# Kernel tuning notes

Hardware: AMD Instinct MI355X
Metric: run time of the kernel (lower is better)

The kernel has to match this reference:

```python
import jax, jax.numpy as jnp
import numpy as np

B = 1024
P = 9            # patch_length
D = 2700         # d_model = input_dims = 30*30*3, num_heads=1 so d_k = D
DFF = 512
EPS = 1e-5


def setup_inputs() -> dict:
    key = jax.random.key(0)
    ks = jax.random.split(key, 32)
    s = 0.02
    inp = {
        "state": jax.random.normal(ks[0], (B, P * D), jnp.float32),
        "H1": jax.random.normal(ks[1], (B, P, DFF), jnp.float32),
        "H2": jax.random.normal(ks[2], (B, P, DFF), jnp.float32),
        # main projections: (in, out) layout for x @ W
        "Wq": jax.random.normal(ks[3], (D, D), jnp.float32) * s,
        "bq": jnp.zeros((D,), jnp.float32),
        "Wk": jax.random.normal(ks[4], (D, D), jnp.float32) * s,
        "bk": jnp.zeros((D,), jnp.float32),
        "Wv": jax.random.normal(ks[5], (D, D), jnp.float32) * s,
        "bv": jnp.zeros((D,), jnp.float32),
        # aux modulation projections from dff -> d_model
        "WC1q": jax.random.normal(ks[6], (DFF, D), jnp.float32) * s,
        "bC1q": jnp.zeros((D,), jnp.float32),
        "WC1k": jax.random.normal(ks[7], (DFF, D), jnp.float32) * s,
        "bC1k": jnp.zeros((D,), jnp.float32),
        "WC1v": jax.random.normal(ks[8], (DFF, D), jnp.float32) * s,
        "bC1v": jnp.zeros((D,), jnp.float32),
        "WC2q": jax.random.normal(ks[9], (DFF, D), jnp.float32) * s,
        "bC2q": jnp.zeros((D,), jnp.float32),
        "WC2k": jax.random.normal(ks[10], (DFF, D), jnp.float32) * s,
        "bC2k": jnp.zeros((D,), jnp.float32),
        "WC2v": jax.random.normal(ks[11], (DFF, D), jnp.float32) * s,
        "bC2v": jnp.zeros((D,), jnp.float32),
        # LayerNorm (norm1) affine params
        "gamma": jnp.ones((D,), jnp.float32),
        "beta": jnp.zeros((D,), jnp.float32),
    }
    return inp


def _layernorm(x, gamma, beta):
    mu = jnp.mean(x, axis=-1, keepdims=True)
    var = jnp.mean(jnp.square(x - mu), axis=-1, keepdims=True)
    return (x - mu) * jax.lax.rsqrt(var + EPS) * gamma + beta


def reference(state, H1, H2, Wq, bq, Wk, bk, Wv, bv,
              WC1q, bC1q, WC1k, bC1k, WC1v, bC1v,
              WC2q, bC2q, WC2k, bC2k, WC2v, bC2v,
              gamma, beta):
    x = state.reshape(-1, P, D)  # (B, 9, 2700)
    # elementwise-modulated Q/K/V (num_heads == 1)
    q = (x @ Wq + bq) * ((H1 @ WC1q + bC1q) + (H2 @ WC2q + bC2q))
    k = (x @ Wk + bk) * ((H1 @ WC1k + bC1k) + (H2 @ WC2k + bC2k))
    v = (x @ Wv + bv) * ((H1 @ WC1v + bC1v) + (H2 @ WC2v + bC2v))
    scale = 1.0 / jnp.sqrt(jnp.asarray(D, jnp.float32))
    scores = jnp.einsum("bqd,bkd->bqk", q, k) * scale  # (B, 9, 9)
    A = jax.nn.softmax(scores, axis=-1)
    attn = jnp.einsum("bqk,bkd->bqd", A, v)
    Z1 = x + attn  # dropout is identity in eval
    return _layernorm(Z1, gamma, beta)
```

## Files before the change

### kernel.cpp

```cpp
#include <hip/hip_runtime.h>
#include <stdint.h>


#define MROWS  9216
#define NCOLS  8192
#define KP1    2752
#define KP2    1024
#define DMODEL 2700

typedef __bf16 bf16x8 __attribute__((ext_vector_type(8)));
typedef float  f32x4  __attribute__((ext_vector_type(4)));

__device__ __forceinline__ float b2f(unsigned short u) {
  union { unsigned int u; float f; } v; v.u = ((unsigned int)u) << 16; return v.f;
}
__device__ __forceinline__ unsigned short f2b(float f) {
  union { float f; unsigned int u; } v; v.f = f;
  unsigned int r = v.u + 0x7FFFu + ((v.u >> 16) & 1u);
  return (unsigned short)(r >> 16);
}

__device__ __forceinline__ void gl2lds16(const void* g, void* l) {
  __builtin_amdgcn_global_load_lds(
      (const __attribute__((address_space(1))) void*)g,
      (__attribute__((address_space(3))) void*)l, 16, 0, 0);
}


__global__ void cvt_x(const float* __restrict__ src, unsigned short* __restrict__ dst) {
  int t = blockIdx.x * 256 + threadIdx.x;
  int r = t / 344;
  int c8 = (t - r * 344) * 8;
  const float* row = src + (size_t)r * DMODEL;
  unsigned int w[4];
  if (c8 + 8 <= DMODEL) {
    float4 a = *(const float4*)(row + c8);
    float4 b = *(const float4*)(row + c8 + 4);
    w[0] = (unsigned int)f2b(a.x) | ((unsigned int)f2b(a.y) << 16);
    w[1] = (unsigned int)f2b(a.z) | ((unsigned int)f2b(a.w) << 16);
    w[2] = (unsigned int)f2b(b.x) | ((unsigned int)f2b(b.y) << 16);
    w[3] = (unsigned int)f2b(b.z) | ((unsigned int)f2b(b.w) << 16);
  } else {
#pragma unroll
    for (int h = 0; h < 4; h++) {
      int c0 = c8 + 2 * h, c1 = c8 + 2 * h + 1;
      unsigned int lo = (c0 < DMODEL) ? f2b(row[c0]) : 0u;
      unsigned int hi = (c1 < DMODEL) ? f2b(row[c1]) : 0u;
      w[h] = lo | (hi << 16);
    }
  }
  *(uint4*)(dst + (size_t)t * 8) = make_uint4(w[0], w[1], w[2], w[3]);
}

__global__ void cvt_h(const float* __restrict__ H1, const float* __restrict__ H2,
                      unsigned short* __restrict__ dst) {
  int t = blockIdx.x * 256 + threadIdx.x;
  int r = t >> 7, c8 = (t & 127) * 8;
  const float* row = (c8 < 512) ? (H1 + (size_t)r * 512 + c8)
                                : (H2 + (size_t)r * 512 + (c8 - 512));
  float4 a = *(const float4*)(row);
  float4 b = *(const float4*)(row + 4);
  unsigned int w0 = (unsigned int)f2b(a.x) | ((unsigned int)f2b(a.y) << 16);
  unsigned int w1 = (unsigned int)f2b(a.z) | ((unsigned int)f2b(a.w) << 16);
  unsigned int w2 = (unsigned int)f2b(b.x) | ((unsigned int)f2b(b.y) << 16);
  unsigned int w3 = (unsigned int)f2b(b.z) | ((unsigned int)f2b(b.w) << 16);
  *(uint4*)(dst + (size_t)t * 8) = make_uint4(w0, w1, w2, w3);
}

__global__ void cvt_wqkv(const float* __restrict__ Wq, const float* __restrict__ Wk,
                         const float* __restrict__ Wv, unsigned short* __restrict__ Wt) {
  __shared__ float tile[64][65];
  const int k0 = blockIdx.x * 64;
  const int n0 = blockIdx.y * 64;
  const int tx = threadIdx.x & 63, tg = threadIdx.x >> 6;
  const int nn_r = n0 + tx;
  int sec = (nn_r >= 5400) ? 2 : ((nn_r >= 2700) ? 1 : 0);
  int d = nn_r - sec * DMODEL;
  const float* W = (sec == 0) ? Wq : ((sec == 1) ? Wk : Wv);
  bool cvalid = (nn_r < 3 * DMODEL);
#pragma unroll
  for (int rr = 0; rr < 16; rr++) {
    int kk = k0 + tg * 16 + rr;
    float v = 0.f;
    if (kk < DMODEL && cvalid) v = W[(size_t)kk * DMODEL + d];
    tile[tg * 16 + rr][tx] = v;
  }
  __syncthreads();
#pragma unroll
  for (int rr = 0; rr < 16; rr++) {
    int nn = n0 + tg * 16 + rr;
    Wt[(size_t)nn * KP1 + k0 + tx] = f2b(tile[tx][tg * 16 + rr]);
  }
}

__global__ void cvt_wc(const float* __restrict__ C1q, const float* __restrict__ C1k,
                       const float* __restrict__ C1v, const float* __restrict__ C2q,
                       const float* __restrict__ C2k, const float* __restrict__ C2v,
                       unsigned short* __restrict__ Wt) {
  __shared__ float tile[64][65];
  const int k0 = blockIdx.x * 64;
  const int n0 = blockIdx.y * 64;
  const int tx = threadIdx.x & 63, tg = threadIdx.x >> 6;
  const int nn_r = n0 + tx;
  int sec = (nn_r >= 5400) ? 2 : ((nn_r >= 2700) ? 1 : 0);
  int d = nn_r - sec * DMODEL;
  bool cvalid = (nn_r < 3 * DMODEL);
  const float* W1 = (sec == 0) ? C1q : ((sec == 1) ? C1k : C1v);
  const float* W2 = (sec == 0) ? C2q : ((sec == 1) ? C2k : C2v);
#pragma unroll
  for (int rr = 0; rr < 16; rr++) {
    int kk = k0 + tg * 16 + rr;
    const float* W = (kk < 512) ? W1 : W2;
    int kr = (kk < 512) ? kk : (kk - 512);
    float v = cvalid ? W[(size_t)kr * DMODEL + d] : 0.f;
    tile[tg * 16 + rr][tx] = v;
  }
  __syncthreads();
#pragma unroll
  for (int rr = 0; rr < 16; rr++) {
    int nn = n0 + tg * 16 + rr;
    Wt[(size_t)nn * KP2 + k0 + tx] = f2b(tile[tx][tg * 16 + rr]);
  }
}

__global__ __launch_bounds__(256, 2) void gemm_fused(
    const unsigned short* __restrict__ Xb,
    const unsigned short* __restrict__ Wt,
    const unsigned short* __restrict__ Hb,
    const unsigned short* __restrict__ WCt,
    unsigned short* __restrict__ MQ,
    const float* __restrict__ bq_, const float* __restrict__ bk_, const float* __restrict__ bv_,
    const float* __restrict__ b1q, const float* __restrict__ b1k, const float* __restrict__ b1v,
    const float* __restrict__ b2q, const float* __restrict__ b2k, const float* __restrict__ b2v)
{
  __shared__ __align__(16) unsigned short As[128 * 64];
  __shared__ __align__(16) unsigned short Bs[128 * 64];
  const int tid = threadIdx.x;
  const int wave = tid >> 6, lane = tid & 63;
  const int m0 = blockIdx.y * 128, n0 = blockIdx.x * 128;
  const int wm = (wave >> 1) * 64, wn = (wave & 1) * 64;
  const int lm = lane & 15, lq = lane >> 4, l7 = lane & 7;

  int prow[4], pcl[4];
  unsigned int ldsoff[4];
#pragma unroll
  for (int r = 0; r < 4; r++) {
    int p = r * 256 + tid;
    prow[r] = p >> 3;
    pcl[r] = ((p & 7) ^ (prow[r] & 7)) * 8;
    ldsoff[r] = (unsigned int)p * 8;
  }

  f32x4 acc[4][4];
#pragma unroll
  for (int i = 0; i < 4; i++)
#pragma unroll
    for (int j = 0; j < 4; j++) acc[i][j] = (f32x4){0.f, 0.f, 0.f, 0.f};

  for (int k0 = 0; k0 < KP2; k0 += 64) {
#pragma unroll
    for (int r = 0; r < 4; r++) {
      gl2lds16(Hb + (size_t)(m0 + prow[r]) * KP2 + pcl[r] + k0, As + ldsoff[r]);
      gl2lds16(WCt + (size_t)(n0 + prow[r]) * KP2 + pcl[r] + k0, Bs + ldsoff[r]);
    }
    __syncthreads();
#pragma unroll
    for (int c = 0; c < 2; c++) {
      bf16x8 af[4], bfr[4];
      const int kx = (c * 4 + lq) ^ l7;
#pragma unroll
      for (int t = 0; t < 4; t++) {
        af[t]  = *(const bf16x8*)(As + (((wm + t * 16 + lm) << 3) + kx) * 8);
        bfr[t] = *(const bf16x8*)(Bs + (((wn + t * 16 + lm) << 3) + kx) * 8);
      }
#pragma unroll
      for (int mt = 0; mt < 4; mt++)
#pragma unroll
        for (int nt = 0; nt < 4; nt++)
          acc[mt][nt] = __builtin_amdgcn_mfma_f32_16x16x32_bf16(
              af[mt], bfr[nt], acc[mt][nt], 0, 0, 0);
    }
    __syncthreads();
  }

  unsigned int modp[4][4][2];
#pragma unroll
  for (int nt = 0; nt < 4; nt++) {
    int gc = n0 + wn + nt * 16 + lm;
    float bmod = 0.f;
    if (gc < 3 * DMODEL) {
      int sec = (gc >= 5400) ? 2 : ((gc >= 2700) ? 1 : 0);
      int d = gc - sec * DMODEL;
      const float* u1 = (sec == 0) ? b1q : ((sec == 1) ? b1k : b1v);
      const float* u2 = (sec == 0) ? b2q : ((sec == 1) ? b2k : b2v);
      bmod = u1[d] + u2[d];
    }
#pragma unroll
    for (int mt = 0; mt < 4; mt++) {
#pragma unroll
      for (int h = 0; h < 2; h++) {
        unsigned int lo = f2b(acc[mt][nt][2 * h] + bmod);
        unsigned int hi = f2b(acc[mt][nt][2 * h + 1] + bmod);
        modp[mt][nt][h] = lo | (hi << 16);
      }
    }
  }
#pragma unroll
  for (int i = 0; i < 4; i++)
#pragma unroll
    for (int j = 0; j < 4; j++) acc[i][j] = (f32x4){0.f, 0.f, 0.f, 0.f};

  for (int k0 = 0; k0 < KP1; k0 += 64) {
#pragma unroll
    for (int r = 0; r < 4; r++) {
      gl2lds16(Xb + (size_t)(m0 + prow[r]) * KP1 + pcl[r] + k0, As + ldsoff[r]);
      gl2lds16(Wt + (size_t)(n0 + prow[r]) * KP1 + pcl[r] + k0, Bs + ldsoff[r]);
    }
    __syncthreads();
#pragma unroll
    for (int c = 0; c < 2; c++) {
      bf16x8 af[4], bfr[4];
      const int kx = (c * 4 + lq) ^ l7;
#pragma unroll
      for (int t = 0; t < 4; t++) {
        af[t]  = *(const bf16x8*)(As + (((wm + t * 16 + lm) << 3) + kx) * 8);
        bfr[t] = *(const bf16x8*)(Bs + (((wn + t * 16 + lm) << 3) + kx) * 8);
      }
#pragma unroll
      for (int mt = 0; mt < 4; mt++)
#pragma unroll
        for (int nt = 0; nt < 4; nt++)
          acc[mt][nt] = __builtin_amdgcn_mfma_f32_16x16x32_bf16(
              af[mt], bfr[nt], acc[mt][nt], 0, 0, 0);
    }
    __syncthreads();
  }

#pragma unroll
  for (int nt = 0; nt < 4; nt++) {
    int gc = n0 + wn + nt * 16 + lm;
    float bmv = 0.f;
    if (gc < 3 * DMODEL) {
      int sec = (gc >= 5400) ? 2 : ((gc >= 2700) ? 1 : 0);
      int d = gc - sec * DMODEL;
      const float* bm = (sec == 0) ? bq_ : ((sec == 1) ? bk_ : bv_);
      bmv = bm[d];
    }
#pragma unroll
    for (int mt = 0; mt < 4; mt++) {
      int grb = m0 + wm + mt * 16 + lq * 4;
#pragma unroll
      for (int i = 0; i < 4; i++) {
        float mod = b2f((unsigned short)(modp[mt][nt][i >> 1] >> ((i & 1) * 16)));
        MQ[(size_t)(grb + i) * NCOLS + gc] = f2b((acc[mt][nt][i] + bmv) * mod);
      }
    }
  }
}

__global__ __launch_bounds__(256, 2) void attn_ln(
    const unsigned short* __restrict__ qkv,
    const float* __restrict__ x,
    const float* __restrict__ gamma, const float* __restrict__ beta,
    float* __restrict__ out)
{
  __shared__ float part[4][81];
  __shared__ float sc[81];
  __shared__ float redS[4][9], redQ[4][9];
  __shared__ float muL[9], rsL[9];

  const int b = blockIdx.x;
  const int tid = threadIdx.x, wave = tid >> 6, lane = tid & 63;
  const unsigned short* qb = qkv + (size_t)b * 9 * NCOLS;

  {
    const int l15 = lane & 15, lq8 = (lane >> 4) * 8;
    const int rA = (l15 < 9) ? l15 : 8;
    const unsigned short* qrow = qb + (size_t)rA * NCOLS;
    const unsigned short* krow = qb + (size_t)rA * NCOLS + DMODEL;
    f32x4 accS = (f32x4){0.f, 0.f, 0.f, 0.f};
    for (int s = wave; s < 85; s += 4) {
      int k0 = s * 32 + lq8;
      union { uint2 u[2]; unsigned int w[4]; bf16x8 v; } au, bu;
      au.u[0] = *(const uint2*)(qrow + k0);
      au.u[1] = *(const uint2*)(qrow + k0 + 4);
      bu.u[0] = *(const uint2*)(krow + k0);
      bu.u[1] = *(const uint2*)(krow + k0 + 4);
      if (s == 84) {
#pragma unroll
        for (int wd = 0; wd < 4; wd++)
          if (k0 + 2 * wd >= DMODEL) { au.w[wd] = 0u; bu.w[wd] = 0u; }
      }
      accS = __builtin_amdgcn_mfma_f32_16x16x32_bf16(au.v, bu.v, accS, 0, 0, 0);
    }
#pragma unroll
    for (int i = 0; i < 4; i++) {
      int row = (lane >> 4) * 4 + i, col = l15;
      if (row < 9 && col < 9) part[wave][row * 9 + col] = accS[i];
    }
  }
  __syncthreads();

  if (tid < 81)
    sc[tid] = (part[0][tid] + part[1][tid] + part[2][tid] + part[3][tid])
              * 0.019245008972987526f;
  __syncthreads();

  if (tid < 9) {
    float mx = -1e30f;
#pragma unroll
    for (int j = 0; j < 9; j++) mx = fmaxf(mx, sc[tid * 9 + j]);
    float e[9], sum = 0.f;
#pragma unroll
    for (int j = 0; j < 9; j++) { e[j] = __expf(sc[tid * 9 + j] - mx); sum += e[j]; }
    float inv = 1.f / sum;
#pragma unroll
    for (int j = 0; j < 9; j++) sc[tid * 9 + j] = e[j] * inv;
  }
  __syncthreads();

  float sum[9], sq[9];
#pragma unroll
  for (int i = 0; i < 9; i++) { sum[i] = 0.f; sq[i] = 0.f; }
  unsigned int pv[9][3][2];
#pragma unroll
  for (int c = 0; c < 3; c++) {
    int e = tid + c * 256;
    if (e < 675) {
      float4 t4[9];
#pragma unroll
      for (int i = 0; i < 9; i++)
        t4[i] = ((const float4*)(x + (size_t)(b * 9 + i) * DMODEL))[e];
#pragma unroll
      for (int j = 0; j < 9; j++) {
        ushort4 vv = ((const ushort4*)(qb + (size_t)j * NCOLS + 5400))[e];
        float v0 = b2f(vv.x), v1 = b2f(vv.y), v2 = b2f(vv.z), v3 = b2f(vv.w);
#pragma unroll
        for (int i = 0; i < 9; i++) {
          float p = sc[i * 9 + j];
          t4[i].x += p * v0; t4[i].y += p * v1;
          t4[i].z += p * v2; t4[i].w += p * v3;
        }
      }
#pragma unroll
      for (int i = 0; i < 9; i++) {
        sum[i] += t4[i].x + t4[i].y + t4[i].z + t4[i].w;
        sq[i]  += t4[i].x * t4[i].x + t4[i].y * t4[i].y
                + t4[i].z * t4[i].z + t4[i].w * t4[i].w;
        pv[i][c][0] = (unsigned int)f2b(t4[i].x) | ((unsigned int)f2b(t4[i].y) << 16);
        pv[i][c][1] = (unsigned int)f2b(t4[i].z) | ((unsigned int)f2b(t4[i].w) << 16);
      }
    }
  }

#pragma unroll
  for (int i = 0; i < 9; i++) {
    float s = sum[i], q = sq[i];
#pragma unroll
    for (int off = 32; off > 0; off >>= 1) {
      s += __shfl_down(s, off, 64);
      q += __shfl_down(q, off, 64);
    }
    if (lane == 0) { redS[wave][i] = s; redQ[wave][i] = q; }
  }
  __syncthreads();
  if (tid < 9) {
    float ts = redS[0][tid] + redS[1][tid] + redS[2][tid] + redS[3][tid];
    float tq = redQ[0][tid] + redQ[1][tid] + redQ[2][tid] + redQ[3][tid];
    float mu = ts * (1.f / 2700.f);
    muL[tid] = mu;
    rsL[tid] = rsqrtf(tq * (1.f / 2700.f) - mu * mu + 1e-5f);
  }
  __syncthreads();

#pragma unroll
  for (int c = 0; c < 3; c++) {
    int e = tid + c * 256;
    if (e < 675) {
      float4 g = ((const float4*)gamma)[e];
      float4 bb = ((const float4*)beta)[e];
#pragma unroll
      for (int i = 0; i < 9; i++) {
        float m = muL[i], r = rsL[i];
        float t0 = b2f((unsigned short)(pv[i][c][0] & 0xFFFF));
        float t1 = b2f((unsigned short)(pv[i][c][0] >> 16));
        float t2 = b2f((unsigned short)(pv[i][c][1] & 0xFFFF));
        float t3 = b2f((unsigned short)(pv[i][c][1] >> 16));
        float4 o;
        o.x = (t0 - m) * r * g.x + bb.x;
        o.y = (t1 - m) * r * g.y + bb.y;
        o.z = (t2 - m) * r * g.z + bb.z;
        o.w = (t3 - m) * r * g.w + bb.w;
        ((float4*)(out + (size_t)(b * 9 + i) * DMODEL))[e] = o;
      }
    }
  }
}

extern "C" void kernel_launch(void* const* d_in, const int* in_sizes, int n_in,
                              void* d_out, int out_size, void* d_ws, size_t ws_size,
                              hipStream_t stream) {
  const float* state = (const float*)d_in[0];
  const float* H1    = (const float*)d_in[1];
  const float* H2    = (const float*)d_in[2];
  const float* Wq    = (const float*)d_in[3];
  const float* bq    = (const float*)d_in[4];
  const float* Wk    = (const float*)d_in[5];
  const float* bk    = (const float*)d_in[6];
  const float* Wv    = (const float*)d_in[7];
  const float* bv    = (const float*)d_in[8];
  const float* WC1q  = (const float*)d_in[9];
  const float* bC1q  = (const float*)d_in[10];
  const float* WC1k  = (const float*)d_in[11];
  const float* bC1k  = (const float*)d_in[12];
  const float* WC1v  = (const float*)d_in[13];
  const float* bC1v  = (const float*)d_in[14];
  const float* WC2q  = (const float*)d_in[15];
  const float* bC2q  = (const float*)d_in[16];
  const float* WC2k  = (const float*)d_in[17];
  const float* bC2k  = (const float*)d_in[18];
  const float* WC2v  = (const float*)d_in[19];
  const float* bC2v  = (const float*)d_in[20];
  const float* gamma = (const float*)d_in[21];
  const float* beta  = (const float*)d_in[22];
  float* out = (float*)d_out;

  char* ws = (char*)d_ws;
  unsigned short* Xb  = (unsigned short*)(ws + 0);
  unsigned short* Wt  = (unsigned short*)(ws + 50724864);
  unsigned short* Hb  = (unsigned short*)(ws + 95813632);
  unsigned short* WCt = (unsigned short*)(ws + 114688000);
  unsigned short* MQ  = (unsigned short*)(ws + 131465216);

  cvt_x<<<dim3(12384), dim3(256), 0, stream>>>(state, Xb);
  cvt_wqkv<<<dim3(43, 128), dim3(256), 0, stream>>>(Wq, Wk, Wv, Wt);
  cvt_h<<<dim3(4608), dim3(256), 0, stream>>>(H1, H2, Hb);
  cvt_wc<<<dim3(16, 128), dim3(256), 0, stream>>>(WC1q, WC1k, WC1v,
                                                  WC2q, WC2k, WC2v, WCt);

  gemm_fused<<<dim3(NCOLS / 128, MROWS / 128), dim3(256), 0, stream>>>(
      Xb, Wt, Hb, WCt, MQ, bq, bk, bv, bC1q, bC1k, bC1v, bC2q, bC2k, bC2v);

  attn_ln<<<dim3(1024), dim3(256), 0, stream>>>(MQ, state, gamma, beta, out);
}
```

Baseline: 1.079 ms.

## Pipeline fused GEMM with triple-buffered LDS, 256x128 tiles and swizzled block order

Replaces the synchronous single-buffer GEMM loop with a triple-buffered LDS pipeline. Global-to-LDS loads run two k-steps ahead and are interleaved with MFMA bursts, gated by explicit vmcnt waits and raw barriers. Blocks grow to 512 threads computing 256x128 tiles on a 1D grid with a swizzled tile order for L2 locality, and bias loads are hoisted before the main loops. This aims to hide memory latency behind MFMAs, at the cost of 144KB of LDS (one block per CU) and fragile hand-set wait counts.

Result: slower. 1.715 ms (+58.9%).

```diff
diff --git a/kernel.cpp b/kernel.cpp
--- a/kernel.cpp
+++ b/kernel.cpp
@@ -25,6 +25,8 @@
       (const __attribute__((address_space(1))) void*)g,
       (__attribute__((address_space(3))) void*)l, 16, 0, 0);
 }
+
+#define BAR() __builtin_amdgcn_s_barrier()
 
 
 __global__ void cvt_x(const float* __restrict__ src, unsigned short* __restrict__ dst) {
@@ -123,7 +125,69 @@
   }
 }
 
-__global__ __launch_bounds__(256, 2) void gemm_fused(
+template<int NT, int KS>
+__device__ __forceinline__ void pipe_gemm(
+    unsigned short (&lds)[3][24576],
+    const unsigned short* Aptr,
+    const unsigned short* Bptr,
+    f32x4 (&acc)[4][4],
+    int tid, int wm, int wn, int lm, int lq, int l7)
+{
+  auto stA = [&](int buf, int u, int t) {
+    gl2lds16(Aptr + (size_t)u * 64 * KS + (size_t)t * 64,
+             &lds[buf][(u * 512 + tid) * 8]);
+  };
+  auto stB = [&](int buf, int u, int t) {
+    gl2lds16(Bptr + (size_t)u * 64 * KS + (size_t)t * 64,
+             &lds[buf][16384 + (u * 512 + tid) * 8]);
+  };
+  bf16x8 af[4], bfr[4];
+  auto frags = [&](int buf, int c) {
+    const int kx = ((c * 4 + lq) ^ l7) * 8;
+#pragma unroll
+    for (int i = 0; i < 4; i++) {
+      af[i]  = *(const bf16x8*)&lds[buf][(wm + i * 16 + lm) * 64 + kx];
+      bfr[i] = *(const bf16x8*)&lds[buf][16384 + (wn + i * 16 + lm) * 64 + kx];
+    }
+  };
+  auto mfmas = [&]() {
+    asm volatile("s_waitcnt lgkmcnt(0)" ::: "memory");
+    __builtin_amdgcn_sched_barrier(0);
+    __builtin_amdgcn_s_setprio(1);
+#pragma unroll
+    for (int mt = 0; mt < 4; mt++)
+#pragma unroll
+      for (int nt = 0; nt < 4; nt++)
+        acc[mt][nt] = __builtin_amdgcn_mfma_f32_16x16x32_bf16(
+            af[mt], bfr[nt], acc[mt][nt], 0, 0, 0);
+    __builtin_amdgcn_s_setprio(0);
+  };
+
+  stA(0, 0, 0); stA(0, 1, 0); stB(0, 0, 0);
+  stA(0, 2, 0); stA(0, 3, 0); stB(0, 1, 0);
+  stA(1, 0, 1); stA(1, 1, 1); stB(1, 0, 1);
+  stA(1, 2, 1); stA(1, 3, 1); stB(1, 1, 1);
+
+  int buf = 0, bpre = 2;
+#pragma unroll 1
+  for (int t = 0; t < NT; ++t) {
+    if (t + 1 < NT) asm volatile("s_waitcnt vmcnt(6)" ::: "memory");
+    else            asm volatile("s_waitcnt vmcnt(0)" ::: "memory");
+    BAR();
+    const bool pre = (t + 2 < NT);
+    if (pre) { stA(bpre, 0, t + 2); stA(bpre, 1, t + 2); stB(bpre, 0, t + 2); }
+    frags(buf, 0);
+    mfmas();
+    if (pre) { stA(bpre, 2, t + 2); stA(bpre, 3, t + 2); stB(bpre, 1, t + 2); }
+    frags(buf, 1);
+    mfmas();
+    BAR();
+    buf  = (buf  == 2) ? 0 : buf  + 1;
+    bpre = (bpre == 2) ? 0 : bpre + 1;
+  }
+}
+
+__global__ void gemm_pipe(
     const unsigned short* __restrict__ Xb,
     const unsigned short* __restrict__ Wt,
     const unsigned short* __restrict__ Hb,
@@ -133,74 +197,59 @@
     const float* __restrict__ b1q, const float* __restrict__ b1k, const float* __restrict__ b1v,
     const float* __restrict__ b2q, const float* __restrict__ b2k, const float* __restrict__ b2v)
 {
-  __shared__ __align__(16) unsigned short As[128 * 64];
-  __shared__ __align__(16) unsigned short Bs[128 * 64];
+  __shared__ __attribute__((aligned(16))) unsigned short lds[3][24576];
   const int tid = threadIdx.x;
   const int wave = tid >> 6, lane = tid & 63;
-  const int m0 = blockIdx.y * 128, n0 = blockIdx.x * 128;
   const int wm = (wave >> 1) * 64, wn = (wave & 1) * 64;
   const int lm = lane & 15, lq = lane >> 4, l7 = lane & 7;
-
-  int prow[4], pcl[4];
-  unsigned int ldsoff[4];
-#pragma unroll
-  for (int r = 0; r < 4; r++) {
-    int p = r * 256 + tid;
-    prow[r] = p >> 3;
-    pcl[r] = ((p & 7) ^ (prow[r] & 7)) * 8;
-    ldsoff[r] = (unsigned int)p * 8;
-  }
-
-  f32x4 acc[4][4];
-#pragma unroll
-  for (int i = 0; i < 4; i++)
-#pragma unroll
-    for (int j = 0; j < 4; j++) acc[i][j] = (f32x4){0.f, 0.f, 0.f, 0.f};
-
-  for (int k0 = 0; k0 < KP2; k0 += 64) {
-#pragma unroll
-    for (int r = 0; r < 4; r++) {
-      gl2lds16(Hb + (size_t)(m0 + prow[r]) * KP2 + pcl[r] + k0, As + ldsoff[r]);
-      gl2lds16(WCt + (size_t)(n0 + prow[r]) * KP2 + pcl[r] + k0, Bs + ldsoff[r]);
-    }
-    __syncthreads();
-#pragma unroll
-    for (int c = 0; c < 2; c++) {
-      bf16x8 af[4], bfr[4];
-      const int kx = (c * 4 + lq) ^ l7;
-#pragma unroll
-      for (int t = 0; t < 4; t++) {
-        af[t]  = *(const bf16x8*)(As + (((wm + t * 16 + lm) << 3) + kx) * 8);
-        bfr[t] = *(const bf16x8*)(Bs + (((wn + t * 16 + lm) << 3) + kx) * 8);
-      }
-#pragma unroll
-      for (int mt = 0; mt < 4; mt++)
-#pragma unroll
-        for (int nt = 0; nt < 4; nt++)
-          acc[mt][nt] = __builtin_amdgcn_mfma_f32_16x16x32_bf16(
-              af[mt], bfr[nt], acc[mt][nt], 0, 0, 0);
-    }
-    __syncthreads();
-  }
-
-  unsigned int modp[4][4][2];
+  const int wg = blockIdx.x;
+  const int swz = (wg & 7) * 288 + (wg >> 3);
+  const int m0 = (swz >> 6) * 256;
+  const int n0 = (swz & 63) * 128;
+  const int sr = tid >> 3;
+  const int skb = ((tid & 7) ^ (sr & 7)) * 8;
+
+  float bmodv[4], bmainv[4];
 #pragma unroll
   for (int nt = 0; nt < 4; nt++) {
     int gc = n0 + wn + nt * 16 + lm;
-    float bmod = 0.f;
+    float vm = 0.f, vb = 0.f;
     if (gc < 3 * DMODEL) {
       int sec = (gc >= 5400) ? 2 : ((gc >= 2700) ? 1 : 0);
       int d = gc - sec * DMODEL;
       const float* u1 = (sec == 0) ? b1q : ((sec == 1) ? b1k : b1v);
       const float* u2 = (sec == 0) ? b2q : ((sec == 1) ? b2k : b2v);
-      bmod = u1[d] + u2[d];
-    }
+      const float* bm = (sec == 0) ? bq_ : ((sec == 1) ? bk_ : bv_);
+      vm = u1[d] + u2[d];
+      vb = bm[d];
+    }
+    bmodv[nt] = vm; bmainv[nt] = vb;
+  }
+  asm volatile("" :: "v"(bmodv[0]), "v"(bmodv[1]), "v"(bmodv[2]), "v"(bmodv[3]),
+                     "v"(bmainv[0]), "v"(bmainv[1]), "v"(bmainv[2]), "v"(bmainv[3]));
+  asm volatile("s_waitcnt vmcnt(0) lgkmcnt(0)" ::: "memory");
+
+  f32x4 acc[4][4];
+#pragma unroll
+  for (int i = 0; i < 4; i++)
+#pragma unroll
+    for (int j = 0; j < 4; j++) acc[i][j] = (f32x4){0.f, 0.f, 0.f, 0.f};
+
+  {
+    const unsigned short* Ap = Hb  + (size_t)(m0 + sr) * KP2 + skb;
+    const unsigned short* Bp = WCt + (size_t)(n0 + sr) * KP2 + skb;
+    pipe_gemm<16, KP2>(lds, Ap, Bp, acc, tid, wm, wn, lm, lq, l7);
+  }
+
+  unsigned int modp[4][4][2];
+#pragma unroll
+  for (int nt = 0; nt < 4; nt++) {
 #pragma unroll
     for (int mt = 0; mt < 4; mt++) {
 #pragma unroll
       for (int h = 0; h < 2; h++) {
-        unsigned int lo = f2b(acc[mt][nt][2 * h] + bmod);
-        unsigned int hi = f2b(acc[mt][nt][2 * h + 1] + bmod);
+        unsigned int lo = f2b(acc[mt][nt][2 * h] + bmodv[nt]);
+        unsigned int hi = f2b(acc[mt][nt][2 * h + 1] + bmodv[nt]);
         modp[mt][nt][h] = lo | (hi << 16);
       }
     }
@@ -210,49 +259,22 @@
 #pragma unroll
     for (int j = 0; j < 4; j++) acc[i][j] = (f32x4){0.f, 0.f, 0.f, 0.f};
 
-  for (int k0 = 0; k0 < KP1; k0 += 64) {
-#pragma unroll
-    for (int r = 0; r < 4; r++) {
-      gl2lds16(Xb + (size_t)(m0 + prow[r]) * KP1 + pcl[r] + k0, As + ldsoff[r]);
-      gl2lds16(Wt + (size_t)(n0 + prow[r]) * KP1 + pcl[r] + k0, Bs + ldsoff[r]);
-    }
-    __syncthreads();
-#pragma unroll
-    for (int c = 0; c < 2; c++) {
-      bf16x8 af[4], bfr[4];
-      const int kx = (c * 4 + lq) ^ l7;
-#pragma unroll
-      for (int t = 0; t < 4; t++) {
-        af[t]  = *(const bf16x8*)(As + (((wm + t * 16 + lm) << 3) + kx) * 8);
-        bfr[t] = *(const bf16x8*)(Bs + (((wn + t * 16 + lm) << 3) + kx) * 8);
-      }
-#pragma unroll
-      for (int mt = 0; mt < 4; mt++)
-#pragma unroll
-        for (int nt = 0; nt < 4; nt++)
-          acc[mt][nt] = __builtin_amdgcn_mfma_f32_16x16x32_bf16(
-              af[mt], bfr[nt], acc[mt][nt], 0, 0, 0);
-    }
-    __syncthreads();
+  {
+    const unsigned short* Ap = Xb + (size_t)(m0 + sr) * KP1 + skb;
+    const unsigned short* Bp = Wt + (size_t)(n0 + sr) * KP1 + skb;
+    pipe_gemm<43, KP1>(lds, Ap, Bp, acc, tid, wm, wn, lm, lq, l7);
   }
 
 #pragma unroll
   for (int nt = 0; nt < 4; nt++) {
     int gc = n0 + wn + nt * 16 + lm;
-    float bmv = 0.f;
-    if (gc < 3 * DMODEL) {
-      int sec = (gc >= 5400) ? 2 : ((gc >= 2700) ? 1 : 0);
-      int d = gc - sec * DMODEL;
-      const float* bm = (sec == 0) ? bq_ : ((sec == 1) ? bk_ : bv_);
-      bmv = bm[d];
-    }
 #pragma unroll
     for (int mt = 0; mt < 4; mt++) {
       int grb = m0 + wm + mt * 16 + lq * 4;
 #pragma unroll
       for (int i = 0; i < 4; i++) {
         float mod = b2f((unsigned short)(modp[mt][nt][i >> 1] >> ((i & 1) * 16)));
-        MQ[(size_t)(grb + i) * NCOLS + gc] = f2b((acc[mt][nt][i] + bmv) * mod);
+        MQ[(size_t)(grb + i) * NCOLS + gc] = f2b((acc[mt][nt][i] + bmainv[nt]) * mod);
       }
     }
   }
@@ -438,7 +460,7 @@
   cvt_wc<<<dim3(16, 128), dim3(256), 0, stream>>>(WC1q, WC1k, WC1v,
                                                   WC2q, WC2k, WC2v, WCt);
 
-  gemm_fused<<<dim3(NCOLS / 128, MROWS / 128), dim3(256), 0, stream>>>(
+  gemm_pipe<<<dim3(2304), dim3(512), 0, stream>>>(
       Xb, Wt, Hb, WCt, MQ, bq, bk, bv, bC1q, bC1k, bC1v, bC2q, bC2k, bC2v);
 
   attn_ln<<<dim3(1024), dim3(256), 0, stream>>>(MQ, state, gamma, beta, out);
```
